# Kernel tuning notes

Hardware: AMD Instinct MI355X
Metric: run time of the kernel (lower is better)

Reference implementation:

```python
import jax, jax.numpy as jnp
import numpy as np

B, N, N_IN, N_HID, N_OUT, T = 64, 64, 64, 256, 64, 4
E = N * (N - 1)  # 4032 directed edges, fully connected minus self-loops


def _incidence():
    # off-diagonal sender/receiver index pairs, NRI-style one-hot matrices
    send_idx, rec_idx = [], []
    for i in range(N):
        for j in range(N):
            if i != j:
                send_idx.append(i)
                rec_idx.append(j)
    eye = np.eye(N, dtype=np.float32)
    rel_send = eye[np.array(send_idx)]  # [E, N]
    rel_rec = eye[np.array(rec_idx)]    # [E, N]
    return jnp.asarray(rel_rec), jnp.asarray(rel_send)


def setup_inputs() -> dict:
    key = jax.random.key(0)
    ks = jax.random.split(key, 16)
    rel_rec, rel_send = _incidence()
    s1 = 1.0 / np.sqrt(2 * N_IN)
    s2 = 1.0 / np.sqrt(N_HID)
    s3 = 1.0 / np.sqrt(N_IN + N_OUT)
    return {
        "x": jax.random.normal(ks[0], (B, N, N_IN), jnp.float32),
        "rel_type": jax.random.uniform(ks[1], (B, E, T), jnp.float32),
        "rel_rec": rel_rec,
        "rel_send": rel_send,
        # per-edge-type message MLPs, stored as [T, in, out] (torch Linear transposed)
        "w1": jax.random.uniform(ks[2], (T, 2 * N_IN, N_HID), jnp.float32, -s1, s1),
        "b1": jax.random.uniform(ks[3], (T, N_HID), jnp.float32, -s1, s1),
        "w2": jax.random.uniform(ks[4], (T, N_HID, N_OUT), jnp.float32, -s2, s2),
        "b2": jax.random.uniform(ks[5], (T, N_OUT), jnp.float32, -s2, s2),
        "ow1": jax.random.uniform(ks[6], (N_IN + N_OUT, N_HID), jnp.float32, -s3, s3),
        "ob1": jax.random.uniform(ks[7], (N_HID,), jnp.float32, -s3, s3),
        "ow2": jax.random.uniform(ks[8], (N_HID, N_HID), jnp.float32, -s2, s2),
        "ob2": jax.random.uniform(ks[9], (N_HID,), jnp.float32, -s2, s2),
        "ow3": jax.random.uniform(ks[10], (N_HID, N_OUT), jnp.float32, -s2, s2),
        "ob3": jax.random.uniform(ks[11], (N_OUT,), jnp.float32, -s2, s2),
    }


def reference(x, rel_type, rel_rec, rel_send, w1, b1, w2, b2, ow1, ob1, ow2, ob2, ow3, ob3):
    # node2edge gather: [E,N] @ [B,N,F] -> [B,E,F]
    receivers = jnp.einsum('en,bnf->bef', rel_rec, x)
    senders = jnp.einsum('en,bnf->bef', rel_send, x)
    pre_msg = jnp.concatenate([senders, receivers], axis=-1)  # [B,E,2F]
    all_msgs = jnp.zeros((pre_msg.shape[0], pre_msg.shape[1], w2.shape[-1]), pre_msg.dtype)
    for i in range(w1.shape[0]):  # small fixed edge_types loop (structurally distinct weights)
        m = jax.nn.relu(pre_msg @ w1[i] + b1[i])           # [B,E,H]
        m = jax.nn.relu(m @ w2[i] + b2[i])                 # [B,E,O]
        all_msgs = all_msgs + m * rel_type[:, :, i:i + 1]  # weighted accumulate
    # edge2node scatter-aggregate: [N,E] @ [B,E,O] -> [B,N,O]
    agg_msgs = jnp.einsum('en,beo->bno', rel_rec, all_msgs)
    aug = jnp.concatenate([x, agg_msgs], axis=-1)          # [B,N,F+O]
    h = jax.nn.relu(aug @ ow1 + ob1)
    h = jax.nn.relu(h @ ow2 + ob2)
    return h @ ow3 + ob3                                   # [B,N,O]
```

## Files before the change

### kernel.cpp

```cpp
#include <hip/hip_runtime.h>

typedef unsigned short u16;
typedef __attribute__((ext_vector_type(8))) _Float16 f16x8;
typedef __attribute__((ext_vector_type(4))) _Float16 f16x4;
typedef __attribute__((ext_vector_type(2))) _Float16 f16x2;
typedef __attribute__((ext_vector_type(4))) float f32x4;

#define DEV static __device__ __forceinline__

DEV float bf2f(u16 h){ unsigned u = ((unsigned)h) << 16; return __builtin_bit_cast(float, u); }
DEV u16 f2bf(float f){ unsigned u = __builtin_bit_cast(unsigned, f); u += 0x7FFFu + ((u >> 16) & 1u); return (u16)(u >> 16); }
DEV u16 f2h(float f){ _Float16 h = (_Float16)f; return __builtin_bit_cast(u16, h); }
DEV float h2f(u16 h){ return (float)__builtin_bit_cast(_Float16, h); }

DEV f32x4 mfma16(f16x8 a, f16x8 b, f32x4 c){
  return __builtin_amdgcn_mfma_f32_16x16x32_f16(a, b, c, 0, 0, 0);
}

DEV unsigned rap(unsigned a, unsigned b){
  f16x2 ha = __builtin_bit_cast(f16x2, a);
  f16x2 hb = __builtin_bit_cast(f16x2, b);
  f16x2 s = ha + hb;
  const _Float16 z = (_Float16)0;
  s.x = s.x > z ? s.x : z;
  s.y = s.y > z ? s.y : z;
  return __builtin_bit_cast(unsigned, s);
}

DEV f16x8 build_frag(uint4 s, uint4 r){
  uint4 o;
  o.x = rap(s.x, r.x); o.y = rap(s.y, r.y);
  o.z = rap(s.z, r.z); o.w = rap(s.w, r.w);
  return __builtin_bit_cast(f16x8, o);
}

#define OFF_W1T  256
#define OFF_W2T  262400
#define OFF_OW1T 393472
#define OFF_OW2T 459008
#define OFF_OW3T 590080
#define OFF_B1   622848
#define OFF_B2   624896
#define OFF_OB1  625408
#define OFF_OB2  625920
#define OFF_OB3  626432
#define OFF_S1   626688
#define OFF_R1   9015296
#define OFF_AGG  17403904
#define OFF_RTT  18452480

DEV float ldin(const void* p, int i, int isbf){
  return isbf ? bf2f(((const u16*)p)[i]) : ((const float*)p)[i];
}

DEV int sniff_isbf(const u16* x, int tid, int* sflag){
  if(tid < 64){
    u16 u = x[2 * tid];
    int e = (u >> 7) & 0xFF;
    int ok = (e >= 103 && e <= 143) ? 1 : 0;
    unsigned long long m = __ballot(ok);
    if(tid == 0) *sflag = (__builtin_popcountll(m) >= 40) ? 1 : 0;
  }
  __syncthreads();
  return *sflag;
}

__global__ __launch_bounds__(256) void k_prep(const void* __restrict__ x, const void* __restrict__ rt,
    const void* __restrict__ w1, const void* __restrict__ b1,
    const void* __restrict__ w2, const void* __restrict__ b2,
    const void* __restrict__ ow1, const void* __restrict__ ob1,
    const void* __restrict__ ow2, const void* __restrict__ ob2,
    const void* __restrict__ ow3, const void* __restrict__ ob3,
    char* __restrict__ ws){
  __shared__ float tile[32][33];
  __shared__ u16 sT[16384];
  __shared__ int sflag;
  const int bid = blockIdx.x, tid = threadIdx.x;
  const int isbf = sniff_isbf((const u16*)x, tid, &sflag);
  if(bid >= 313){
    const int b = bid - 313;
    uint4 zz; zz.x = zz.y = zz.z = zz.w = 0;
    #pragma unroll
    for(int it=0; it<8; ++it) ((uint4*)sT)[tid + it*256] = zz;
    __syncthreads();
    #pragma unroll 1
    for(int it=0; it<16; ++it){
      int e = tid + it*256;
      if(e < 4032){
        int i = e / 63, jr = e - i*63;
        int j = jr + (jr >= i ? 1 : 0);
        u16 w[4];
        if(isbf){
          ushort4 v = *(const ushort4*)((const u16*)rt + b*16128 + e*4);
          w[0] = f2h(bf2f(v.x)); w[1] = f2h(bf2f(v.y));
          w[2] = f2h(bf2f(v.z)); w[3] = f2h(bf2f(v.w));
        } else {
          float4 v = *(const float4*)((const float*)rt + b*16128 + e*4);
          w[0] = f2h(v.x); w[1] = f2h(v.y); w[2] = f2h(v.z); w[3] = f2h(v.w);
        }
        #pragma unroll
        for(int tt=0; tt<4; ++tt) sT[(tt*64 + j)*64 + i] = w[tt];
      }
    }
    __syncthreads();
    u16* RTT = (u16*)(ws + OFF_RTT);
    #pragma unroll
    for(int tt=0; tt<4; ++tt){
      uint4* dst = (uint4*)(RTT + ((tt*64 + b)*64)*64);
      const uint4* srcv = (const uint4*)(sT + tt*4096);
      #pragma unroll
      for(int it=0; it<2; ++it){
        int c = tid + it*256;
        dst[c] = srcv[c];
      }
    }
    return;
  }
  if(bid == 312){ if(tid == 0) *(int*)ws = isbf; return; }
  if(bid >= 304){
    int n = (bid - 304) * 256 + tid;
    if(n < 1024){ ((u16*)(ws+OFF_B1))[n] = f2h(ldin(b1, n, isbf)); return; }
    n -= 1024;
    if(n < 256){ ((u16*)(ws+OFF_B2))[n] = f2h(ldin(b2, n, isbf)); return; }
    n -= 256;
    if(n < 256){ ((u16*)(ws+OFF_OB1))[n] = f2h(ldin(ob1, n, isbf)); return; }
    n -= 256;
    if(n < 256){ ((u16*)(ws+OFF_OB2))[n] = f2h(ldin(ob2, n, isbf)); return; }
    n -= 256;
    if(n < 64){ ((u16*)(ws+OFF_OB3))[n] = f2h(ldin(ob3, n, isbf)); }
    return;
  }
  const void* src; u16* dst; int R, C, off, r0, c0;
  if(bid < 128){ int g = bid >> 5, tt = bid & 31;
    src = w1; dst = (u16*)(ws + OFF_W1T); R = 128; C = 256; off = g * 32768;
    r0 = (tt >> 3) << 5; c0 = (tt & 7) << 5;
  } else if(bid < 192){ int bb = bid - 128; int g = bb >> 4, tt = bb & 15;
    src = w2; dst = (u16*)(ws + OFF_W2T); R = 256; C = 64; off = g * 16384;
    r0 = (tt >> 1) << 5; c0 = (tt & 1) << 5;
  } else if(bid < 224){ int bb = bid - 192;
    src = ow1; dst = (u16*)(ws + OFF_OW1T); R = 128; C = 256; off = 0;
    r0 = (bb >> 3) << 5; c0 = (bb & 7) << 5;
  } else if(bid < 288){ int bb = bid - 224;
    src = ow2; dst = (u16*)(ws + OFF_OW2T); R = 256; C = 256; off = 0;
    r0 = (bb >> 3) << 5; c0 = (bb & 7) << 5;
  } else { int bb = bid - 288;
    src = ow3; dst = (u16*)(ws + OFF_OW3T); R = 256; C = 64; off = 0;
    r0 = (bb >> 1) << 5; c0 = (bb & 1) << 5;
  }
  int tx = tid & 31, ty = tid >> 5;
  #pragma unroll
  for(int p = 0; p < 4; ++p){
    int r = ty + p * 8;
    tile[r][tx] = ldin(src, off + (r0 + r) * C + c0 + tx, isbf);
  }
  __syncthreads();
  #pragma unroll
  for(int p = 0; p < 4; ++p){
    int c = ty + p * 8;
    dst[off + (c0 + c) * R + r0 + tx] = f2h(tile[tx][c]);
  }
}

__global__ __launch_bounds__(256) void k_s1r1(const void* __restrict__ x, const u16* __restrict__ W1T,
    const u16* __restrict__ B1c, u16* __restrict__ S1, u16* __restrict__ R1,
    float* __restrict__ AGG, const int* __restrict__ flag){
  __shared__ __align__(16) u16 sX[64][72];
  __shared__ __align__(16) u16 sW[256][72];
  const int tid = threadIdx.x, bid = blockIdx.x;
  const int b = bid & 63, th = bid >> 6, t = th >> 1, half = th & 1;
  const int isbf = *flag;
  {
    float2 zz; zz.x = 0.f; zz.y = 0.f;
    ((float2*)AGG)[bid*256 + tid] = zz;
  }
  {
    if(isbf){
      const uint4* src = (const uint4*)((const u16*)x + b*4096);
      #pragma unroll
      for(int it=0; it<2; ++it){
        int c = tid + it*256; int row = c >> 3, col = (c & 7) * 8;
        uint4 v = src[c];
        const u16* pv = (const u16*)&v;
        u16 o[8];
        #pragma unroll
        for(int e=0;e<8;++e) o[e] = f2h(bf2f(pv[e]));
        *(uint4*)&sX[row][col] = *(const uint4*)o;
      }
    } else {
      const float* src = (const float*)x + b*4096;
      #pragma unroll
      for(int it=0; it<2; ++it){
        int c = tid + it*256; int row = c >> 3, col = (c & 7) * 8;
        u16 o[8];
        #pragma unroll
        for(int e=0;e<8;++e) o[e] = f2h(src[c*8 + e]);
        *(uint4*)&sX[row][col] = *(const uint4*)o;
      }
    }
    const u16* base = W1T + t*32768 + half*64;
    #pragma unroll
    for(int it=0; it<8; ++it){
      int c = tid + it*256; int h = c >> 3, kc = (c & 7) * 8;
      *(uint4*)&sW[h][kc] = *(const uint4*)(base + h*128 + kc);
    }
  }
  __syncthreads();
  const int wv = tid >> 6, l = tid & 63, ml = l & 15, q = l >> 4;
  const f32x4 z = {0.f,0.f,0.f,0.f};
  f32x4 acc[4][4];
  #pragma unroll
  for(int mt=0;mt<4;++mt){ acc[mt][0]=z; acc[mt][1]=z; acc[mt][2]=z; acc[mt][3]=z; }
  #pragma unroll
  for(int ks=0; ks<2; ++ks){
    const int kb = ks*32 + q*8;
    f16x8 af[4], bff[4];
    #pragma unroll
    for(int mt=0;mt<4;++mt) af[mt] = *(const f16x8*)&sX[mt*16 + ml][kb];
    #pragma unroll
    for(int nt=0;nt<4;++nt) bff[nt] = *(const f16x8*)&sW[wv*64 + nt*16 + ml][kb];
    #pragma unroll
    for(int mt=0;mt<4;++mt)
      #pragma unroll
      for(int nt=0;nt<4;++nt)
        acc[mt][nt] = mfma16(af[mt], bff[nt], acc[mt][nt]);
  }
  u16* dst = (half ? R1 : S1) + (t*64 + b)*16384;
  #pragma unroll
  for(int nt=0;nt<4;++nt){
    const int h = wv*64 + nt*16 + ml;
    const float bias = half ? h2f(B1c[t*256 + h]) : 0.0f;
    #pragma unroll
    for(int mt=0;mt<4;++mt)
      #pragma unroll
      for(int r=0;r<4;++r){
        int irow = mt*16 + q*4 + r;
        dst[irow*256 + h] = f2h(acc[mt][nt][r] + bias);
      }
  }
}

__global__ __launch_bounds__(256, 2) void k_edge(const u16* __restrict__ RTT,
    const u16* __restrict__ W2T, const u16* __restrict__ B2c,
    const u16* __restrict__ S1, const u16* __restrict__ R1,
    float* __restrict__ AGG){
  __shared__ __align__(16) u16 sRT[32][64];
  __shared__ float sOut[2048];
  const int tid = threadIdx.x, bid = blockIdx.x;
  const int t = bid >> 7, b = (bid >> 1) & 63, jh = bid & 1, j0 = jh * 32;
  const int w = tid >> 6, l = tid & 63, ml = l & 15, q = l >> 4;
  const int ih = w & 1, oh = w >> 1;
  #pragma unroll
  for(int it=0; it<8; ++it) sOut[tid + it*256] = 0.0f;
  ((uint4*)sRT)[tid] = ((const uint4*)(RTT + ((t*64 + b)*64 + j0)*64))[tid];
  __syncthreads();
  uint4 su[2][8];
  f16x8 bf[2][8];
  {
    const u16* s1b = S1 + (t*64 + b)*16384;
    const u16* w2t = W2T + t*16384;
    #pragma unroll
    for(int mt=0;mt<2;++mt)
      #pragma unroll
      for(int ks=0;ks<8;++ks)
        su[mt][ks] = *(const uint4*)(s1b + (ih*32 + mt*16 + ml)*256 + ks*32 + q*8);
    #pragma unroll
    for(int nt=0;nt<2;++nt)
      #pragma unroll
      for(int ks=0;ks<8;++ks)
        bf[nt][ks] = *(const f16x8*)(w2t + (oh*32 + nt*16 + ml)*256 + ks*32 + q*8);
  }
  float bias2[2];
  #pragma unroll
  for(int nt=0;nt<2;++nt) bias2[nt] = h2f(B2c[t*64 + oh*32 + nt*16 + ml]);
  const u16* r1b = R1 + (t*64 + b)*16384 + j0*256;
  const f32x4 z = {0.f,0.f,0.f,0.f};
  #pragma unroll 1
  for(int jl=0; jl<32; ++jl){
    uint4 ru[8];
    {
      const u16* rp = r1b + jl*256;
      #pragma unroll
      for(int ks=0;ks<8;++ks) ru[ks] = *(const uint4*)(rp + ks*32 + q*8);
    }
    f32x4 acc[2][2];
    acc[0][0]=z; acc[0][1]=z; acc[1][0]=z; acc[1][1]=z;
    #pragma unroll
    for(int ks=0;ks<8;++ks){
      #pragma unroll
      for(int mt=0;mt<2;++mt){
        f16x8 af = build_frag(su[mt][ks], ru[ks]);
        acc[mt][0] = mfma16(af, bf[0][ks], acc[mt][0]);
        acc[mt][1] = mfma16(af, bf[1][ks], acc[mt][1]);
      }
    }
    float cs[2] = {0.f, 0.f};
    #pragma unroll
    for(int mt=0;mt<2;++mt){
      f16x4 rv = *(const f16x4*)&sRT[jl][ih*32 + mt*16 + q*4];
      #pragma unroll
      for(int nt=0;nt<2;++nt)
        #pragma unroll
        for(int r=0;r<4;++r)
          cs[nt] += fmaxf(acc[mt][nt][r] + bias2[nt], 0.0f) * (float)rv[r];
    }
    #pragma unroll
    for(int nt=0;nt<2;++nt){
      float v = cs[nt];
      v += __shfl_xor(v, 16, 64);
      v += __shfl_xor(v, 32, 64);
      if(q == 0) atomicAdd(&sOut[jl*64 + oh*32 + nt*16 + ml], v);
    }
  }
  __syncthreads();
  float* aggp = AGG + (b*64 + j0)*64;
  #pragma unroll
  for(int it=0; it<8; ++it){
    int c = tid + it*256;
    atomicAdd(&aggp[c], sOut[c]);
  }
}

__global__ __launch_bounds__(256) void k_n1(const void* __restrict__ x, const float* __restrict__ AGG,
    const u16* __restrict__ OW1T, const u16* __restrict__ OB1c,
    u16* __restrict__ H, const int* __restrict__ flag){
  __shared__ __align__(16) u16 sA[64][136];
  __shared__ __align__(16) u16 sW[64][136];
  const int tid = threadIdx.x, bb = blockIdx.x & 63, nc = blockIdx.x >> 6;
  const int isbf = *flag;
  {
    if(isbf){
      const uint4* src = (const uint4*)((const u16*)x + bb*4096);
      #pragma unroll
      for(int it=0; it<2; ++it){
        int c = tid + it*256; int row = c >> 3, col = (c & 7)*8;
        uint4 v = src[c];
        const u16* pv = (const u16*)&v;
        u16 o[8];
        #pragma unroll
        for(int e=0;e<8;++e) o[e] = f2h(bf2f(pv[e]));
        *(uint4*)&sA[row][col] = *(const uint4*)o;
      }
    } else {
      const float* src = (const float*)x + bb*4096;
      #pragma unroll
      for(int it=0; it<2; ++it){
        int c = tid + it*256; int row = c >> 3, col = (c & 7)*8;
        u16 o[8];
        #pragma unroll
        for(int e=0;e<8;++e) o[e] = f2h(src[c*8 + e]);
        *(uint4*)&sA[row][col] = *(const uint4*)o;
      }
    }
    const float* ag = AGG + bb*4096;
    #pragma unroll
    for(int it=0; it<16; ++it){
      int c = tid + it*256; int row = c >> 6, col = c & 63;
      sA[row][64 + col] = f2h(ag[c]);
    }
    #pragma unroll
    for(int it=0; it<4; ++it){
      int c = tid + it*256; int h = c >> 4, kc = (c & 15)*8;
      *(uint4*)&sW[h][kc] = *(const uint4*)(OW1T + (nc*64 + h)*128 + kc);
    }
  }
  const int wv = tid >> 6, l = tid & 63, ml = l & 15, q = l >> 4;
  const f32x4 z = {0.f,0.f,0.f,0.f};
  __syncthreads();
  f32x4 acc[4] = {z,z,z,z};
  #pragma unroll
  for(int ks=0; ks<4; ++ks){
    int kb = ks*32 + q*8;
    f16x8 bfrag = *(const f16x8*)&sW[wv*16 + ml][kb];
    #pragma unroll
    for(int mt=0;mt<4;++mt){
      f16x8 afrag = *(const f16x8*)&sA[mt*16 + ml][kb];
      acc[mt] = mfma16(afrag, bfrag, acc[mt]);
    }
  }
  const int h = nc*64 + wv*16 + ml;
  const float bias = h2f(OB1c[h]);
  #pragma unroll
  for(int mt=0;mt<4;++mt)
    #pragma unroll
    for(int r=0;r<4;++r){
      int row = mt*16 + q*4 + r;
      H[(bb*64 + row)*256 + h] = f2h(fmaxf(acc[mt][r] + bias, 0.0f));
    }
}

__global__ __launch_bounds__(256) void k_n2(const u16* __restrict__ H,
    const u16* __restrict__ OW2T, const u16* __restrict__ OB2c,
    u16* __restrict__ H2){
  __shared__ __align__(16) u16 sH[64][264];
  __shared__ __align__(16) u16 sW[64][264];
  const int tid = threadIdx.x, bb = blockIdx.x & 63, nc = blockIdx.x >> 6;
  {
    const uint4* hp = (const uint4*)(H + bb*16384);
    #pragma unroll
    for(int it=0; it<8; ++it){
      int c = tid + it*256; int row = c >> 5, col = (c & 31)*8;
      *(uint4*)&sH[row][col] = hp[c];
      *(uint4*)&sW[row][col] = *(const uint4*)(OW2T + nc*16384 + c*8);
    }
  }
  const int wv = tid >> 6, l = tid & 63, ml = l & 15, q = l >> 4;
  const f32x4 z = {0.f,0.f,0.f,0.f};
  __syncthreads();
  f32x4 acc[4] = {z,z,z,z};
  #pragma unroll
  for(int ks=0; ks<8; ++ks){
    int kb = ks*32 + q*8;
    f16x8 bfrag = *(const f16x8*)&sW[wv*16 + ml][kb];
    #pragma unroll
    for(int mt=0;mt<4;++mt){
      f16x8 afrag = *(const f16x8*)&sH[mt*16 + ml][kb];
      acc[mt] = mfma16(afrag, bfrag, acc[mt]);
    }
  }
  const int h = nc*64 + wv*16 + ml;
  const float bias = h2f(OB2c[h]);
  #pragma unroll
  for(int mt=0;mt<4;++mt)
    #pragma unroll
    for(int r=0;r<4;++r){
      int row = mt*16 + q*4 + r;
      H2[(bb*64 + row)*256 + h] = f2h(fmaxf(acc[mt][r] + bias, 0.0f));
    }
}

__global__ __launch_bounds__(256) void k_n3(const u16* __restrict__ H2,
    const u16* __restrict__ OW3T, const u16* __restrict__ OB3c,
    void* __restrict__ out, const int* __restrict__ flag){
  __shared__ __align__(16) u16 sH[64][264];
  __shared__ __align__(16) u16 sW[64][264];
  const int tid = threadIdx.x, bb = blockIdx.x;
  const int isbf = *flag;
  {
    const uint4* hp = (const uint4*)(H2 + bb*16384);
    #pragma unroll
    for(int it=0; it<8; ++it){
      int c = tid + it*256; int row = c >> 5, col = (c & 31)*8;
      *(uint4*)&sH[row][col] = hp[c];
      *(uint4*)&sW[row][col] = *(const uint4*)(OW3T + c*8);
    }
  }
  const int wv = tid >> 6, l = tid & 63, ml = l & 15, q = l >> 4;
  const f32x4 z = {0.f,0.f,0.f,0.f};
  __syncthreads();
  f32x4 acc[4] = {z,z,z,z};
  #pragma unroll
  for(int ks=0; ks<8; ++ks){
    int kb = ks*32 + q*8;
    f16x8 bfrag = *(const f16x8*)&sW[wv*16 + ml][kb];
    #pragma unroll
    for(int mt=0;mt<4;++mt){
      f16x8 afrag = *(const f16x8*)&sH[mt*16 + ml][kb];
      acc[mt] = mfma16(afrag, bfrag, acc[mt]);
    }
  }
  const int o = wv*16 + ml;
  const float bias = h2f(OB3c[o]);
  #pragma unroll
  for(int mt=0;mt<4;++mt)
    #pragma unroll
    for(int r=0;r<4;++r){
      int row = mt*16 + q*4 + r;
      float v = acc[mt][r] + bias;
      int idx = bb*4096 + row*64 + o;
      if(isbf) ((u16*)out)[idx] = f2bf(v);
      else     ((float*)out)[idx] = v;
    }
}

extern "C" void kernel_launch(void* const* d_in, const int* in_sizes, int n_in,
                              void* d_out, int out_size, void* d_ws, size_t ws_size,
                              hipStream_t stream){
  (void)in_sizes; (void)n_in; (void)out_size; (void)ws_size;
  char* ws = (char*)d_ws;
  u16* W1T  = (u16*)(ws + OFF_W1T);
  u16* W2T  = (u16*)(ws + OFF_W2T);
  u16* OW1T = (u16*)(ws + OFF_OW1T);
  u16* OW2T = (u16*)(ws + OFF_OW2T);
  u16* OW3T = (u16*)(ws + OFF_OW3T);
  u16* B1c  = (u16*)(ws + OFF_B1);
  u16* B2c  = (u16*)(ws + OFF_B2);
  u16* OB1c = (u16*)(ws + OFF_OB1);
  u16* OB2c = (u16*)(ws + OFF_OB2);
  u16* OB3c = (u16*)(ws + OFF_OB3);
  u16* S1   = (u16*)(ws + OFF_S1);
  u16* R1   = (u16*)(ws + OFF_R1);
  float* AGG = (float*)(ws + OFF_AGG);
  u16* RTT  = (u16*)(ws + OFF_RTT);
  u16* H    = (u16*)(ws + OFF_S1);
  u16* H2   = (u16*)(ws + OFF_R1);
  const int* flag = (const int*)ws;

  k_prep<<<377, 256, 0, stream>>>(d_in[0], d_in[1], d_in[4], d_in[5], d_in[6], d_in[7],
                                  d_in[8], d_in[9], d_in[10], d_in[11], d_in[12], d_in[13], ws);
  k_s1r1<<<512, 256, 0, stream>>>(d_in[0], W1T, B1c, S1, R1, AGG, flag);
  k_edge<<<512, 256, 0, stream>>>(RTT, W2T, B2c, S1, R1, AGG);
  k_n1<<<256, 256, 0, stream>>>(d_in[0], AGG, OW1T, OB1c, H, flag);
  k_n2<<<256, 256, 0, stream>>>(H, OW2T, OB2c, H2);
  k_n3<<<64, 256, 0, stream>>>(H2, OW3T, OB3c, d_out, flag);
}
```

Measured before the change: 193.3 us.

## Repartition edge kernel so each wave owns whole receiver rows, W2 staged in LDS

In the edge kernel, each wave now computes a full 64x64 tile (all senders and all outputs) for its own set of 8 receivers. Previously the four waves split the sender and output dimensions and shared every receiver. Because each receiver's output row is written by one wave, the shared-memory atomics and zero-init of sOut become plain stores. W2 is copied into padded LDS and read per k-step instead of being held in registers, and the S1 fragment held per wave doubles. The min-blocks-per-CU hint is dropped, which likely raises register use and lowers occupancy, and adds LDS traffic for W2.

```diff
diff --git a/kernel.cpp b/kernel.cpp
--- a/kernel.cpp
+++ b/kernel.cpp
@@ -239,76 +239,82 @@
   }
 }
 
-__global__ __launch_bounds__(256, 2) void k_edge(const u16* __restrict__ RTT,
+__global__ __launch_bounds__(256) void k_edge(const u16* __restrict__ RTT,
     const u16* __restrict__ W2T, const u16* __restrict__ B2c,
     const u16* __restrict__ S1, const u16* __restrict__ R1,
     float* __restrict__ AGG){
+  __shared__ __align__(16) u16 sW2[64][264];
   __shared__ __align__(16) u16 sRT[32][64];
   __shared__ float sOut[2048];
   const int tid = threadIdx.x, bid = blockIdx.x;
   const int t = bid >> 7, b = (bid >> 1) & 63, jh = bid & 1, j0 = jh * 32;
+  {
+    const uint4* w2p = (const uint4*)(W2T + t*16384);
+    #pragma unroll
+    for(int it=0; it<8; ++it){
+      int c = tid + it*256;
+      int row = c >> 5, col = (c & 31) * 8;
+      *(uint4*)&sW2[row][col] = w2p[c];
+    }
+    ((uint4*)sRT)[tid] = ((const uint4*)(RTT + ((t*64 + b)*64 + j0)*64))[tid];
+  }
+  __syncthreads();
   const int w = tid >> 6, l = tid & 63, ml = l & 15, q = l >> 4;
-  const int ih = w & 1, oh = w >> 1;
-  #pragma unroll
-  for(int it=0; it<8; ++it) sOut[tid + it*256] = 0.0f;
-  ((uint4*)sRT)[tid] = ((const uint4*)(RTT + ((t*64 + b)*64 + j0)*64))[tid];
-  __syncthreads();
-  uint4 su[2][8];
-  f16x8 bf[2][8];
+  uint4 su[4][8];
   {
     const u16* s1b = S1 + (t*64 + b)*16384;
-    const u16* w2t = W2T + t*16384;
-    #pragma unroll
-    for(int mt=0;mt<2;++mt)
+    #pragma unroll
+    for(int mt=0;mt<4;++mt)
       #pragma unroll
       for(int ks=0;ks<8;++ks)
-        su[mt][ks] = *(const uint4*)(s1b + (ih*32 + mt*16 + ml)*256 + ks*32 + q*8);
-    #pragma unroll
-    for(int nt=0;nt<2;++nt)
-      #pragma unroll
-      for(int ks=0;ks<8;++ks)
-        bf[nt][ks] = *(const f16x8*)(w2t + (oh*32 + nt*16 + ml)*256 + ks*32 + q*8);
-  }
-  float bias2[2];
-  #pragma unroll
-  for(int nt=0;nt<2;++nt) bias2[nt] = h2f(B2c[t*64 + oh*32 + nt*16 + ml]);
+        su[mt][ks] = *(const uint4*)(s1b + (mt*16 + ml)*256 + ks*32 + q*8);
+  }
+  float bias2[4];
+  #pragma unroll
+  for(int nt=0;nt<4;++nt) bias2[nt] = h2f(B2c[t*64 + nt*16 + ml]);
   const u16* r1b = R1 + (t*64 + b)*16384 + j0*256;
   const f32x4 z = {0.f,0.f,0.f,0.f};
   #pragma unroll 1
-  for(int jl=0; jl<32; ++jl){
+  for(int jp=0; jp<8; ++jp){
+    const int jl = w*8 + jp;
     uint4 ru[8];
     {
       const u16* rp = r1b + jl*256;
       #pragma unroll
       for(int ks=0;ks<8;++ks) ru[ks] = *(const uint4*)(rp + ks*32 + q*8);
     }
-    f32x4 acc[2][2];
-    acc[0][0]=z; acc[0][1]=z; acc[1][0]=z; acc[1][1]=z;
+    f32x4 acc[4][4];
+    #pragma unroll
+    for(int mt=0;mt<4;++mt){ acc[mt][0]=z; acc[mt][1]=z; acc[mt][2]=z; acc[mt][3]=z; }
     #pragma unroll
     for(int ks=0;ks<8;++ks){
-      #pragma unroll
-      for(int mt=0;mt<2;++mt){
+      const int kb = ks*32 + q*8;
+      f16x8 bf[4];
+      #pragma unroll
+      for(int nt=0;nt<4;++nt) bf[nt] = *(const f16x8*)&sW2[nt*16 + ml][kb];
+      #pragma unroll
+      for(int mt=0;mt<4;++mt){
         f16x8 af = build_frag(su[mt][ks], ru[ks]);
-        acc[mt][0] = mfma16(af, bf[0][ks], acc[mt][0]);
-        acc[mt][1] = mfma16(af, bf[1][ks], acc[mt][1]);
-      }
-    }
-    float cs[2] = {0.f, 0.f};
-    #pragma unroll
-    for(int mt=0;mt<2;++mt){
-      f16x4 rv = *(const f16x4*)&sRT[jl][ih*32 + mt*16 + q*4];
-      #pragma unroll
-      for(int nt=0;nt<2;++nt)
+        #pragma unroll
+        for(int nt=0;nt<4;++nt) acc[mt][nt] = mfma16(af, bf[nt], acc[mt][nt]);
+      }
+    }
+    float cs[4] = {0.f,0.f,0.f,0.f};
+    #pragma unroll
+    for(int mt=0;mt<4;++mt){
+      f16x4 rv = *(const f16x4*)&sRT[jl][mt*16 + q*4];
+      #pragma unroll
+      for(int nt=0;nt<4;++nt)
         #pragma unroll
         for(int r=0;r<4;++r)
           cs[nt] += fmaxf(acc[mt][nt][r] + bias2[nt], 0.0f) * (float)rv[r];
     }
     #pragma unroll
-    for(int nt=0;nt<2;++nt){
+    for(int nt=0;nt<4;++nt){
       float v = cs[nt];
       v += __shfl_xor(v, 16, 64);
       v += __shfl_xor(v, 32, 64);
-      if(q == 0) atomicAdd(&sOut[jl*64 + oh*32 + nt*16 + ml], v);
+      if(q == 0) sOut[jl*64 + nt*16 + ml] = v;
     }
   }
   __syncthreads();
```

New measurement: 180.9 us. 1.07x faster.
